# Kernel optimization log

Hardware: AMD Instinct MI355X
Metric: run time of the kernel (lower is better)

## Reference

```python
import jax, jax.numpy as jnp
import numpy as np

IN_FEATS, H_FEATS, OUT_FEATS = 128, 256, 64
N_NODES, N_EDGES = 50000, 800000
DROP_P = 0.5


def setup_inputs() -> dict:
    key = jax.random.key(0)
    k_h, k_e, k_w1, k_w2 = jax.random.split(key, 4)
    h = jax.random.normal(k_h, (N_NODES, IN_FEATS), dtype=jnp.float32)
    edge_index = jax.random.randint(k_e, (2, N_EDGES), 0, N_NODES, dtype=jnp.int64)
    # Glorot-style init for GraphConv weights; bias zeros (DGL default)
    W1 = jax.random.normal(k_w1, (IN_FEATS, H_FEATS), dtype=jnp.float32) / np.sqrt(IN_FEATS)
    b1 = jnp.zeros((H_FEATS,), dtype=jnp.float32)
    W2 = jax.random.normal(k_w2, (H_FEATS, OUT_FEATS), dtype=jnp.float32) / np.sqrt(H_FEATS)
    b2 = jnp.zeros((OUT_FEATS,), dtype=jnp.float32)
    return {"h": h, "W1": W1, "b1": b1, "W2": W2, "b2": b2,
            "edge_index": edge_index, "n_nodes": N_NODES}


def _sym_norm(edge_index, n_nodes):
    # symmetric GCN norm: deg^-1/2 on both endpoints (in-degree, clamped to 1)
    dst = edge_index[1]
    deg = jax.ops.segment_sum(jnp.ones(edge_index.shape[1], jnp.float32), dst,
                              num_segments=n_nodes)
    return jnp.where(deg > 0, deg, 1.0) ** -0.5  # [N]


def _graph_conv(h, W, b, src, dst, norm, n_nodes, apply_w_first):
    # DGL GraphConv (norm='both'): scale by src norm, aggregate, scale by dst norm.
    # W is applied before aggregation if in_feats > out_feats, else after.
    x = h * norm[:, None]
    if apply_w_first:
        x = x @ W
    agg = jax.ops.segment_sum(x[src], dst, num_segments=n_nodes)
    if not apply_w_first:
        agg = agg @ W
    return agg * norm[:, None] + b


def reference(h, W1, b1, W2, b2, edge_index, n_nodes):
    src, dst = edge_index[0], edge_index[1]
    norm = _sym_norm(edge_index, n_nodes)
    # layer 1: in(128) <= out(256) -> aggregate then transform; relu activation
    h1 = jax.nn.relu(_graph_conv(h, W1, b1, src, dst, norm, n_nodes, apply_w_first=False))
    # dropout(0.5), training mode, deterministic key
    keep = jax.random.bernoulli(jax.random.key(42), 1.0 - DROP_P, h1.shape)
    h1 = jnp.where(keep, h1 / (1.0 - DROP_P), 0.0)
    # layer 2: in(256) > out(64) -> transform then aggregate; no activation
    out = _graph_conv(h1, W2, b2, src, dst, norm, n_nodes, apply_w_first=True)
    return out
```

## Files before the change

kernel.cpp:

```cpp
#include <hip/hip_runtime.h>
#include <stdint.h>

#define N_IN  128
#define N_H   256
#define N_OUT 64
#define CHK   2048
#define CAP   6144

typedef __attribute__((ext_vector_type(8))) __bf16 bf16x8;
typedef __attribute__((ext_vector_type(4))) float f32x4;

__device__ __forceinline__ void tf4(uint32_t& x0, uint32_t& x1,
                                    const int r0, const int r1, const int r2, const int r3) {
  x0 += x1; x1 = (x1 << r0) | (x1 >> (32 - r0)); x1 ^= x0;
  x0 += x1; x1 = (x1 << r1) | (x1 >> (32 - r1)); x1 ^= x0;
  x0 += x1; x1 = (x1 << r2) | (x1 >> (32 - r2)); x1 ^= x0;
  x0 += x1; x1 = (x1 << r3) | (x1 >> (32 - r3)); x1 ^= x0;
}

__device__ __forceinline__ uint2 threefry2x32(uint32_t k0, uint32_t k1, uint32_t x0, uint32_t x1) {
  const uint32_t k2 = k0 ^ k1 ^ 0x1BD11BDAu;
  x0 += k0; x1 += k1;
  tf4(x0, x1, 13, 15, 26, 6);   x0 += k1; x1 += k2 + 1u;
  tf4(x0, x1, 17, 29, 16, 24);  x0 += k2; x1 += k0 + 2u;
  tf4(x0, x1, 13, 15, 26, 6);   x0 += k0; x1 += k1 + 3u;
  tf4(x0, x1, 17, 29, 16, 24);  x0 += k1; x1 += k2 + 4u;
  tf4(x0, x1, 13, 15, 26, 6);   x0 += k2; x1 += k0 + 5u;
  return make_uint2(x0, x1);
}

__device__ __forceinline__ uint16_t f2bf_rne(float v) {
  uint32_t b = __builtin_bit_cast(uint32_t, v);
  b += 0x7fffu + ((b >> 16) & 1u);
  return (uint16_t)(b >> 16);
}
__device__ __forceinline__ float bflo(uint32_t w) { return __builtin_bit_cast(float, w << 16); }
__device__ __forceinline__ float bfhi(uint32_t w) { return __builtin_bit_cast(float, w & 0xffff0000u); }

__device__ __forceinline__ void packW_body(const float* __restrict__ W,
                                           uint4* __restrict__ WH, uint4* __restrict__ WL,
                                           int Ncols, int nct, int nks, int g) {
  if (g >= nct * nks * 64) return;
  int lane = g & 63;
  int grp = g >> 6;
  int ks = grp % nks, ct = grp / nks;
  int k0 = ks * 32 + (lane >> 4) * 8;
  int col = ct * 16 + (lane & 15);
  uint32_t hb[8], lb[8];
#pragma unroll
  for (int j = 0; j < 8; j++) {
    float w = W[(size_t)(k0 + j) * Ncols + col];
    uint32_t bits = __builtin_bit_cast(uint32_t, w);
    uint32_t hi = bits & 0xffff0000u;
    float lo = w - __builtin_bit_cast(float, hi);
    hb[j] = hi >> 16;
    lb[j] = __builtin_bit_cast(uint32_t, lo) >> 16;
  }
  WH[g] = make_uint4(hb[0] | (hb[1] << 16), hb[2] | (hb[3] << 16),
                     hb[4] | (hb[5] << 16), hb[6] | (hb[7] << 16));
  WL[g] = make_uint4(lb[0] | (lb[1] << 16), lb[2] | (lb[3] << 16),
                     lb[4] | (lb[5] << 16), lb[6] | (lb[7] << 16));
}

__global__ __launch_bounds__(256) void k_front(
    const int* __restrict__ eidx, int E, int* __restrict__ bktCur, uint2* __restrict__ eb,
    uint16_t* __restrict__ mask, int N,
    const float* __restrict__ W1, uint4* __restrict__ W1H, uint4* __restrict__ W1L,
    const float* __restrict__ W2, uint4* __restrict__ W2H, uint4* __restrict__ W2L,
    int NBE) {
  const int b = blockIdx.x, t = threadIdx.x;
  if (b < NBE) {
    __shared__ int s_nz;
    __shared__ int hist[256];
    __shared__ int base[256];
    if (t == 0) s_nz = 0;
    hist[t] = 0;
    __syncthreads();
    int n = E < 2048 ? E : 2048;
    int nz = 0;
    for (int i = t; i < n; i += 256) nz |= (eidx[2 * i + 1] != 0) ? 1 : 0;
    if (nz) atomicAdd(&s_nz, 1);
    __syncthreads();
    int stride = (s_nz == 0) ? 2 : 1;

    int cb = b * CHK;
    int dc[8], sc[8];
#pragma unroll
    for (int i = 0; i < 8; i++) {
      int e = cb + i * 256 + t;
      if (e < E) {
        dc[i] = eidx[(size_t)(E + e) * stride];
        sc[i] = eidx[(size_t)e * stride];
        atomicAdd(&hist[dc[i] >> 8], 1);
      } else dc[i] = -1;
    }
    __syncthreads();
    int hcnt = hist[t];
    if (hcnt) base[t] = atomicAdd(&bktCur[t], hcnt);
    __syncthreads();
    hist[t] = 0;
    __syncthreads();
#pragma unroll
    for (int i = 0; i < 8; i++) {
      if (dc[i] >= 0) {
        int bk = dc[i] >> 8;
        int r = atomicAdd(&hist[bk], 1);
        eb[(size_t)bk * CAP + base[bk] + r] = make_uint2((unsigned)sc[i], (unsigned)dc[i]);
      }
    }
  } else {
    const int NBM = (N * 16 + 255) >> 8;
    int bb = b - NBE;
    if (bb < NBM) {
      int g = bb * 256 + t;
      if (g >= N * 16) return;
      uint32_t row = (uint32_t)(g >> 4), colb = (uint32_t)(g & 15);
      uint32_t bse = row * 256u + colb;
      uint32_t m = 0;
#pragma unroll
      for (int ct = 0; ct < 16; ct++) {
        uint2 o = threefry2x32(0u, 42u, 0u, bse + (uint32_t)ct * 16u);
        uint32_t bits = o.x ^ o.y;
        m |= ((~bits) >> 31) << ct;
      }
      mask[g] = (uint16_t)m;
    } else if (bb < NBM + 16) {
      packW_body(W1, W1H, W1L, N_H, 16, 4, (bb - NBM) * 256 + t);
    } else {
      packW_body(W2, W2H, W2L, N_OUT, 4, 8, (bb - NBM - 16) * 256 + t);
    }
  }
}

__global__ __launch_bounds__(256) void k_bucket_csr(
    const uint2* __restrict__ eb, const int* __restrict__ bktCur,
    int* __restrict__ rowptr, float* __restrict__ norm,
    int* __restrict__ esrc, int N, int E) {
  __shared__ int s[256];
  __shared__ int cnt[256];
  __shared__ int pfx[256];
  __shared__ int cur[256];
  const int b = blockIdx.x, t = threadIdx.x;
  if (b == 0 && t == 0) rowptr[N] = E;
  if (b * 256 >= N) return;
  int xc = bktCur[t];
  s[t] = xc;
  __syncthreads();
  for (int off = 1; off < 256; off <<= 1) {
    int u = (t >= off) ? s[t - off] : 0;
    __syncthreads();
    s[t] += u;
    __syncthreads();
  }
  const int lo = (b > 0) ? s[b - 1] : 0;
  const int ecnt = s[b] - lo;
  const uint2* ebb = eb + (size_t)b * CAP;
  cnt[t] = 0;
  __syncthreads();
  for (int e = t; e < ecnt; e += 256)
    atomicAdd(&cnt[ebb[e].y & 255u], 1);
  __syncthreads();
  int x = cnt[t];
  pfx[t] = x;
  __syncthreads();
  for (int off = 1; off < 256; off <<= 1) {
    int u = (t >= off) ? pfx[t - off] : 0;
    __syncthreads();
    pfx[t] += u;
    __syncthreads();
  }
  int excl = pfx[t] - x;
  int node = b * 256 + t;
  if (node < N) {
    rowptr[node] = lo + excl;
    norm[node] = x > 0 ? rsqrtf((float)x) : 1.0f;
  }
  cur[t] = excl;
  __syncthreads();
  for (int e = t; e < ecnt; e += 256) {
    uint2 r = ebb[e];
    int d = (int)(r.y & 255u);
    int p = atomicAdd(&cur[d], 1);
    esrc[lo + p] = (int)r.x;
  }
}

__global__ __launch_bounds__(256) void k_mid(
    int* __restrict__ esrc, const int* __restrict__ rowptr, int N,
    const float* __restrict__ h, const float* __restrict__ norm,
    uint16_t* __restrict__ hn, int NS) {
  const int b = blockIdx.x, t = threadIdx.x;
  if (b < NS) {
    int node = b * 4 + (t >> 6);
    if (node >= N) return;
    const int lane = t & 63;
    int lo = rowptr[node], hi = rowptr[node + 1], d = hi - lo;
    if (d <= 1) return;
    if (d <= 64) {
      int v = (lane < d) ? esrc[lo + lane] : 0x7fffffff;
#pragma unroll
      for (int k = 2; k <= 64; k <<= 1) {
#pragma unroll
        for (int j = k >> 1; j > 0; j >>= 1) {
          int other = __shfl_xor(v, j);
          bool up = ((lane & k) == 0);
          bool lower = ((lane & j) == 0);
          int mn = min(v, other), mx = max(v, other);
          v = (up == lower) ? mn : mx;
        }
      }
      if (lane < d) esrc[lo + lane] = v;
    } else if (lane == 0) {
      for (int i = lo + 1; i < hi; i++) {
        int v = esrc[i];
        int j = i - 1;
        while (j >= lo && esrc[j] > v) { esrc[j + 1] = esrc[j]; j--; }
        esrc[j + 1] = v;
      }
    }
  } else {
    int g = (b - NS) * 256 + t;
    if (g >= N * 32) return;
    float nr = norm[g >> 5];
    float4 v = *reinterpret_cast<const float4*>(h + (size_t)g * 4);
    ushort4 r;
    r.x = f2bf_rne(v.x * nr);
    r.y = f2bf_rne(v.y * nr);
    r.z = f2bf_rne(v.z * nr);
    r.w = f2bf_rne(v.w * nr);
    *reinterpret_cast<ushort4*>(hn + (size_t)g * 4) = r;
  }
}

__global__ __launch_bounds__(256) void k_pull1(
    const uint16_t* __restrict__ hn, const int* __restrict__ rowptr,
    const int* __restrict__ esrc, uint16_t* __restrict__ aggB, int N) {
  int node = blockIdx.x * 16 + (threadIdx.x >> 4);
  if (node >= N) return;
  int lane = threadIdx.x & 15;
  int lo = rowptr[node], hi = rowptr[node + 1];
  float a[8] = {0,0,0,0,0,0,0,0};
  float b[8] = {0,0,0,0,0,0,0,0};
  int e = lo;
  for (; e + 7 < hi; e += 8) {
    int s0 = esrc[e],     s1 = esrc[e + 1], s2 = esrc[e + 2], s3 = esrc[e + 3];
    int s4 = esrc[e + 4], s5 = esrc[e + 5], s6 = esrc[e + 6], s7 = esrc[e + 7];
    uint4 v0 = *reinterpret_cast<const uint4*>(hn + (size_t)s0 * N_IN + lane * 8);
    uint4 v1 = *reinterpret_cast<const uint4*>(hn + (size_t)s1 * N_IN + lane * 8);
    uint4 v2 = *reinterpret_cast<const uint4*>(hn + (size_t)s2 * N_IN + lane * 8);
    uint4 v3 = *reinterpret_cast<const uint4*>(hn + (size_t)s3 * N_IN + lane * 8);
    uint4 v4 = *reinterpret_cast<const uint4*>(hn + (size_t)s4 * N_IN + lane * 8);
    uint4 v5 = *reinterpret_cast<const uint4*>(hn + (size_t)s5 * N_IN + lane * 8);
    uint4 v6 = *reinterpret_cast<const uint4*>(hn + (size_t)s6 * N_IN + lane * 8);
    uint4 v7 = *reinterpret_cast<const uint4*>(hn + (size_t)s7 * N_IN + lane * 8);
    a[0] += bflo(v0.x); a[1] += bfhi(v0.x); a[2] += bflo(v0.y); a[3] += bfhi(v0.y);
    a[4] += bflo(v0.z); a[5] += bfhi(v0.z); a[6] += bflo(v0.w); a[7] += bfhi(v0.w);
    b[0] += bflo(v1.x); b[1] += bfhi(v1.x); b[2] += bflo(v1.y); b[3] += bfhi(v1.y);
    b[4] += bflo(v1.z); b[5] += bfhi(v1.z); b[6] += bflo(v1.w); b[7] += bfhi(v1.w);
    a[0] += bflo(v2.x); a[1] += bfhi(v2.x); a[2] += bflo(v2.y); a[3] += bfhi(v2.y);
    a[4] += bflo(v2.z); a[5] += bfhi(v2.z); a[6] += bflo(v2.w); a[7] += bfhi(v2.w);
    b[0] += bflo(v3.x); b[1] += bfhi(v3.x); b[2] += bflo(v3.y); b[3] += bfhi(v3.y);
    b[4] += bflo(v3.z); b[5] += bfhi(v3.z); b[6] += bflo(v3.w); b[7] += bfhi(v3.w);
    a[0] += bflo(v4.x); a[1] += bfhi(v4.x); a[2] += bflo(v4.y); a[3] += bfhi(v4.y);
    a[4] += bflo(v4.z); a[5] += bfhi(v4.z); a[6] += bflo(v4.w); a[7] += bfhi(v4.w);
    b[0] += bflo(v5.x); b[1] += bfhi(v5.x); b[2] += bflo(v5.y); b[3] += bfhi(v5.y);
    b[4] += bflo(v5.z); b[5] += bfhi(v5.z); b[6] += bflo(v5.w); b[7] += bfhi(v5.w);
    a[0] += bflo(v6.x); a[1] += bfhi(v6.x); a[2] += bflo(v6.y); a[3] += bfhi(v6.y);
    a[4] += bflo(v6.z); a[5] += bfhi(v6.z); a[6] += bflo(v6.w); a[7] += bfhi(v6.w);
    b[0] += bflo(v7.x); b[1] += bfhi(v7.x); b[2] += bflo(v7.y); b[3] += bfhi(v7.y);
    b[4] += bflo(v7.z); b[5] += bfhi(v7.z); b[6] += bflo(v7.w); b[7] += bfhi(v7.w);
  }
  for (; e < hi; e++) {
    uint4 v0 = *reinterpret_cast<const uint4*>(hn + (size_t)esrc[e] * N_IN + lane * 8);
    a[0] += bflo(v0.x); a[1] += bfhi(v0.x); a[2] += bflo(v0.y); a[3] += bfhi(v0.y);
    a[4] += bflo(v0.z); a[5] += bfhi(v0.z); a[6] += bflo(v0.w); a[7] += bfhi(v0.w);
  }
  uint16_t o[8];
#pragma unroll
  for (int i = 0; i < 8; i++) o[i] = f2bf_rne(a[i] + b[i]);
  *reinterpret_cast<uint4*>(aggB + (size_t)node * N_IN + lane * 8) =
      *reinterpret_cast<const uint4*>(o);
}

__global__ __launch_bounds__(256) void k_gemm12(
    const uint16_t* __restrict__ aggB,
    const uint4* __restrict__ W1H, const uint4* __restrict__ W1L,
    const float* __restrict__ b1, const float* __restrict__ norm,
    const uint16_t* __restrict__ mask,
    const uint4* __restrict__ W2H, const uint4* __restrict__ W2L,
    uint16_t* __restrict__ zbf, int Nn) {
  __shared__ uint16_t h1[64 * 256];
  __shared__ uint4 wlds[2048];
  const int tid = threadIdx.x;
  const int wave = tid >> 6, lane = tid & 63;
  const int row0 = blockIdx.x * 64 + wave * 16;
  const int lrow = lane & 15, lk = lane >> 4;
  int arow = row0 + lrow; if (arow >= Nn) arow = Nn - 1;

  uint4 aq[4];
#pragma unroll
  for (int ks = 0; ks < 4; ks++)
    aq[ks] = *reinterpret_cast<const uint4*>(aggB + (size_t)arow * N_IN + ks * 32 + lk * 8);

  f32x4 acc[16];
#pragma unroll
  for (int c = 0; c < 16; c++) acc[c] = f32x4{0.f, 0.f, 0.f, 0.f};

  for (int ks = 0; ks < 4; ks++) {
    __syncthreads();
#pragma unroll
    for (int i = 0; i < 4; i++) {
      int g = tid + i * 256;
      int src = ((g >> 6) * 4 + ks) * 64 + (g & 63);
      wlds[g]        = W1H[src];
      wlds[1024 + g] = W1L[src];
    }
    __syncthreads();
    union { uint4 q; bf16x8 v; } ah; ah.q = aq[ks];
#pragma unroll
    for (int c = 0; c < 16; c++) {
      union { uint4 q; bf16x8 v; } bh, bl;
      bh.q = wlds[c * 64 + lane];
      bl.q = wlds[1024 + c * 64 + lane];
      acc[c] = __builtin_amdgcn_mfma_f32_16x16x32_bf16(ah.v, bh.v, acc[c], 0, 0, 0);
      acc[c] = __builtin_amdgcn_mfma_f32_16x16x32_bf16(ah.v, bl.v, acc[c], 0, 0, 0);
    }
  }

  const int colb = lane & 15, rgrp = lane >> 4;
#pragma unroll
  for (int r = 0; r < 4; r++) {
    int lrw = wave * 16 + rgrp * 4 + r;
    int row = blockIdx.x * 64 + lrw;
    float nr = (row < Nn) ? norm[row] : 0.f;
    uint32_t m = (row < Nn) ? (uint32_t)mask[row * 16 + colb] : 0u;
    int sw = (lrw & 7) << 3;
#pragma unroll
    for (int c = 0; c < 16; c++) {
      int col = c * 16 + colb;
      float v = fmaf(acc[c][r], nr, b1[col]);
      v = fmaxf(v, 0.f);
      v = ((m >> c) & 1u) ? v * (2.0f * nr) : 0.f;
      h1[lrw * 256 + (col ^ sw)] = f2bf_rne(v);
    }
  }

  f32x4 acc2[4];
#pragma unroll
  for (int c = 0; c < 4; c++) acc2[c] = f32x4{0.f, 0.f, 0.f, 0.f};
  const int myrow = wave * 16 + lrow;
  const int sw2 = (myrow & 7) << 3;

  for (int half = 0; half < 2; half++) {
    __syncthreads();
#pragma unroll
    for (int i = 0; i < 4; i++) {
      int g = tid + i * 256;
      int src = ((g >> 8) * 8 + half * 4 + ((g >> 6) & 3)) * 64 + (g & 63);
      wlds[g]        = W2H[src];
      wlds[1024 + g] = W2L[src];
    }
    __syncthreads();
#pragma unroll
    for (int ksl = 0; ksl < 4; ksl++) {
      int ks = half * 4 + ksl;
      union { uint4 q; bf16x8 v; } ah;
      int c0 = (ks * 32 + lk * 8) ^ sw2;
      ah.q = *reinterpret_cast<const uint4*>(&h1[myrow * 256 + c0]);
#pragma unroll
      for (int c = 0; c < 4; c++) {
        union { uint4 q; bf16x8 v; } bh, bl;
        bh.q = wlds[(c * 4 + ksl) * 64 + lane];
        bl.q = wlds[1024 + (c * 4 + ksl) * 64 + lane];
        acc2[c] = __builtin_amdgcn_mfma_f32_16x16x32_bf16(ah.v, bh.v, acc2[c], 0, 0, 0);
        acc2[c] = __builtin_amdgcn_mfma_f32_16x16x32_bf16(ah.v, bl.v, acc2[c], 0, 0, 0);
      }
    }
  }
#pragma unroll
  for (int r = 0; r < 4; r++) {
    int row = row0 + rgrp * 4 + r;
    if (row >= Nn) continue;
#pragma unroll
    for (int c = 0; c < 4; c++)
      zbf[(size_t)row * N_OUT + c * 16 + colb] = f2bf_rne(acc2[c][r]);
  }
}

__global__ __launch_bounds__(256) void k_pull2(
    const uint16_t* __restrict__ zbf, const float* __restrict__ norm,
    const float* __restrict__ b2, const int* __restrict__ rowptr,
    const int* __restrict__ esrc, float* __restrict__ out, int N) {
  int node = blockIdx.x * 32 + (threadIdx.x >> 3);
  if (node >= N) return;
  int lane = threadIdx.x & 7;
  int lo = rowptr[node], hi = rowptr[node + 1];
  float a[8] = {0,0,0,0,0,0,0,0};
  float b[8] = {0,0,0,0,0,0,0,0};
  int e = lo;
  for (; e + 7 < hi; e += 8) {
    int s0 = esrc[e],     s1 = esrc[e + 1], s2 = esrc[e + 2], s3 = esrc[e + 3];
    int s4 = esrc[e + 4], s5 = esrc[e + 5], s6 = esrc[e + 6], s7 = esrc[e + 7];
    uint4 v0 = *reinterpret_cast<const uint4*>(zbf + (size_t)s0 * N_OUT + lane * 8);
    uint4 v1 = *reinterpret_cast<const uint4*>(zbf + (size_t)s1 * N_OUT + lane * 8);
    uint4 v2 = *reinterpret_cast<const uint4*>(zbf + (size_t)s2 * N_OUT + lane * 8);
    uint4 v3 = *reinterpret_cast<const uint4*>(zbf + (size_t)s3 * N_OUT + lane * 8);
    uint4 v4 = *reinterpret_cast<const uint4*>(zbf + (size_t)s4 * N_OUT + lane * 8);
    uint4 v5 = *reinterpret_cast<const uint4*>(zbf + (size_t)s5 * N_OUT + lane * 8);
    uint4 v6 = *reinterpret_cast<const uint4*>(zbf + (size_t)s6 * N_OUT + lane * 8);
    uint4 v7 = *reinterpret_cast<const uint4*>(zbf + (size_t)s7 * N_OUT + lane * 8);
    a[0] += bflo(v0.x); a[1] += bfhi(v0.x); a[2] += bflo(v0.y); a[3] += bfhi(v0.y);
    a[4] += bflo(v0.z); a[5] += bfhi(v0.z); a[6] += bflo(v0.w); a[7] += bfhi(v0.w);
    b[0] += bflo(v1.x); b[1] += bfhi(v1.x); b[2] += bflo(v1.y); b[3] += bfhi(v1.y);
    b[4] += bflo(v1.z); b[5] += bfhi(v1.z); b[6] += bflo(v1.w); b[7] += bfhi(v1.w);
    a[0] += bflo(v2.x); a[1] += bfhi(v2.x); a[2] += bflo(v2.y); a[3] += bfhi(v2.y);
    a[4] += bflo(v2.z); a[5] += bfhi(v2.z); a[6] += bflo(v2.w); a[7] += bfhi(v2.w);
    b[0] += bflo(v3.x); b[1] += bfhi(v3.x); b[2] += bflo(v3.y); b[3] += bfhi(v3.y);
    b[4] += bflo(v3.z); b[5] += bfhi(v3.z); b[6] += bflo(v3.w); b[7] += bfhi(v3.w);
    a[0] += bflo(v4.x); a[1] += bfhi(v4.x); a[2] += bflo(v4.y); a[3] += bfhi(v4.y);
    a[4] += bflo(v4.z); a[5] += bfhi(v4.z); a[6] += bflo(v4.w); a[7] += bfhi(v4.w);
    b[0] += bflo(v5.x); b[1] += bfhi(v5.x); b[2] += bflo(v5.y); b[3] += bfhi(v5.y);
    b[4] += bflo(v5.z); b[5] += bfhi(v5.z); b[6] += bflo(v5.w); b[7] += bfhi(v5.w);
    a[0] += bflo(v6.x); a[1] += bfhi(v6.x); a[2] += bflo(v6.y); a[3] += bfhi(v6.y);
    a[4] += bflo(v6.z); a[5] += bfhi(v6.z); a[6] += bflo(v6.w); a[7] += bfhi(v6.w);
    b[0] += bflo(v7.x); b[1] += bfhi(v7.x); b[2] += bflo(v7.y); b[3] += bfhi(v7.y);
    b[4] += bflo(v7.z); b[5] += bfhi(v7.z); b[6] += bflo(v7.w); b[7] += bfhi(v7.w);
  }
  for (; e < hi; e++) {
    uint4 v0 = *reinterpret_cast<const uint4*>(zbf + (size_t)esrc[e] * N_OUT + lane * 8);
    a[0] += bflo(v0.x); a[1] += bfhi(v0.x); a[2] += bflo(v0.y); a[3] += bfhi(v0.y);
    a[4] += bflo(v0.z); a[5] += bfhi(v0.z); a[6] += bflo(v0.w); a[7] += bfhi(v0.w);
  }
  float nn = norm[node];
  float o[8];
#pragma unroll
  for (int i = 0; i < 8; i++) o[i] = (a[i] + b[i]) * nn + b2[lane * 8 + i];
  *reinterpret_cast<float4*>(out + (size_t)node * N_OUT + lane * 8) =
      make_float4(o[0], o[1], o[2], o[3]);
  *reinterpret_cast<float4*>(out + (size_t)node * N_OUT + lane * 8 + 4) =
      make_float4(o[4], o[5], o[6], o[7]);
}

extern "C" void kernel_launch(void* const* d_in, const int* in_sizes, int n_in,
                              void* d_out, int out_size, void* d_ws, size_t ws_size,
                              hipStream_t stream) {
  const float* h  = (const float*)d_in[0];
  const float* W1 = (const float*)d_in[1];
  const float* b1 = (const float*)d_in[2];
  const float* W2 = (const float*)d_in[3];
  const float* b2 = (const float*)d_in[4];
  const int* eidx = (const int*)d_in[5];
  const int N = in_sizes[0] / N_IN;
  const int E = in_sizes[5] / 2;
  const int NBE = (E + CHK - 1) / CHK;
  const int NBM = (N * 16 + 255) / 256;
  const int NS  = (N + 3) / 4;
  const int NH  = (N * 32 + 255) / 256;

  char* ws = (char*)d_ws;
  size_t off = 0;
  auto alloc = [&](size_t bytes) { void* p = ws + off; off += (bytes + 511) & ~(size_t)511; return p; };
  int*      rowptr = (int*)alloc((size_t)(N + 1) * 4);
  float*    norm   = (float*)alloc((size_t)N * 4);
  int*      esrc   = (int*)alloc((size_t)E * 4);
  int*      bktCur = (int*)alloc((size_t)256 * 4);
  uint16_t* mask   = (uint16_t*)alloc((size_t)N * 16 * 2);
  uint4*    W1H    = (uint4*)alloc((size_t)16 * 4 * 64 * 16);
  uint4*    W1L    = (uint4*)alloc((size_t)16 * 4 * 64 * 16);
  uint4*    W2H    = (uint4*)alloc((size_t)4 * 8 * 64 * 16);
  uint4*    W2L    = (uint4*)alloc((size_t)4 * 8 * 64 * 16);
  uint2*    eb     = (uint2*)alloc((size_t)256 * CAP * 8);
  uint16_t* hn     = (uint16_t*)alloc((size_t)N * N_IN * 2);
  uint16_t* aggB   = (uint16_t*)alloc((size_t)N * N_IN * 2);
  uint16_t* zbf    = (uint16_t*)alloc((size_t)N * N_OUT * 2);
  float*    out    = (float*)d_out;

  hipMemsetAsync(bktCur, 0, 256 * 4, stream);

  k_front<<<NBE + NBM + 16 + 8, 256, 0, stream>>>(eidx, E, bktCur, eb,
                                                  mask, N, W1, W1H, W1L, W2, W2H, W2L, NBE);

  k_bucket_csr<<<256, 256, 0, stream>>>(eb, bktCur, rowptr, norm, esrc, N, E);

  k_mid<<<NS + NH, 256, 0, stream>>>(esrc, rowptr, N, h, norm, hn, NS);

  k_pull1<<<(N + 15) / 16, 256, 0, stream>>>(hn, rowptr, esrc, aggB, N);

  k_gemm12<<<(N + 63) / 64, 256, 0, stream>>>(aggB, W1H, W1L, b1, norm, mask,
                                              W2H, W2L, zbf, N);

  k_pull2<<<(N + 31) / 32, 256, 0, stream>>>(zbf, norm, b2, rowptr, esrc, out, N);
}
```

Before: 146.1 us.

## Fuse per-row edge sort and feature normalization into bucket CSR kernel

Drops the separate k_mid kernel. Each bucket block of k_bucket_csr now sorts its own rows' source lists and writes the normalized bf16 features for its 256 nodes, reading counts and norms from shared memory. This removes one launch and the rowptr/norm reloads from global memory. The cost is that the sort and conversion run on only 256 blocks, one wave per 64 rows serially, rather than across many blocks, so parallelism drops sharply.

After: 205.1 us. +40.3%, slower.

```diff
diff --git a/kernel.cpp b/kernel.cpp
--- a/kernel.cpp
+++ b/kernel.cpp
@@ -135,11 +135,13 @@
 __global__ __launch_bounds__(256) void k_bucket_csr(
     const uint2* __restrict__ eb, const int* __restrict__ bktCur,
     int* __restrict__ rowptr, float* __restrict__ norm,
-    int* __restrict__ esrc, int N, int E) {
+    int* __restrict__ esrc, const float* __restrict__ h,
+    uint16_t* __restrict__ hn, int N, int E) {
   __shared__ int s[256];
   __shared__ int cnt[256];
   __shared__ int pfx[256];
   __shared__ int cur[256];
+  __shared__ float narr[256];
   const int b = blockIdx.x, t = threadIdx.x;
   if (b == 0 && t == 0) rowptr[N] = E;
   if (b * 256 >= N) return;
@@ -171,9 +173,11 @@
   }
   int excl = pfx[t] - x;
   int node = b * 256 + t;
+  float nrm = x > 0 ? rsqrtf((float)x) : 1.0f;
+  narr[t] = nrm;
   if (node < N) {
     rowptr[node] = lo + excl;
-    norm[node] = x > 0 ? rsqrtf((float)x) : 1.0f;
+    norm[node] = nrm;
   }
   cur[t] = excl;
   __syncthreads();
@@ -183,52 +187,55 @@
     int p = atomicAdd(&cur[d], 1);
     esrc[lo + p] = (int)r.x;
   }
-}
-
-__global__ __launch_bounds__(256) void k_mid(
-    int* __restrict__ esrc, const int* __restrict__ rowptr, int N,
-    const float* __restrict__ h, const float* __restrict__ norm,
-    uint16_t* __restrict__ hn, int NS) {
-  const int b = blockIdx.x, t = threadIdx.x;
-  if (b < NS) {
-    int node = b * 4 + (t >> 6);
-    if (node >= N) return;
-    const int lane = t & 63;
-    int lo = rowptr[node], hi = rowptr[node + 1], d = hi - lo;
-    if (d <= 1) return;
+  __syncthreads();
+
+  const int wv = t >> 6, ln = t & 63;
+  const int nrows = min(256, N - b * 256);
+  for (int i = 0; i < 64; i++) {
+    int r = wv * 64 + i;
+    if (r >= nrows) break;
+    int d = cnt[r];
+    if (d <= 1) continue;
+    int rl = lo + pfx[r] - d;
     if (d <= 64) {
-      int v = (lane < d) ? esrc[lo + lane] : 0x7fffffff;
+      int v = (ln < d) ? esrc[rl + ln] : 0x7fffffff;
 #pragma unroll
       for (int k = 2; k <= 64; k <<= 1) {
 #pragma unroll
         for (int j = k >> 1; j > 0; j >>= 1) {
           int other = __shfl_xor(v, j);
-          bool up = ((lane & k) == 0);
-          bool lower = ((lane & j) == 0);
+          bool up = ((ln & k) == 0);
+          bool lower = ((ln & j) == 0);
           int mn = min(v, other), mx = max(v, other);
           v = (up == lower) ? mn : mx;
         }
       }
-      if (lane < d) esrc[lo + lane] = v;
-    } else if (lane == 0) {
-      for (int i = lo + 1; i < hi; i++) {
-        int v = esrc[i];
-        int j = i - 1;
-        while (j >= lo && esrc[j] > v) { esrc[j + 1] = esrc[j]; j--; }
+      if (ln < d) esrc[rl + ln] = v;
+    } else if (ln == 0) {
+      for (int ii = rl + 1; ii < rl + d; ii++) {
+        int v = esrc[ii];
+        int j = ii - 1;
+        while (j >= rl && esrc[j] > v) { esrc[j + 1] = esrc[j]; j--; }
         esrc[j + 1] = v;
       }
     }
-  } else {
-    int g = (b - NS) * 256 + t;
-    if (g >= N * 32) return;
-    float nr = norm[g >> 5];
-    float4 v = *reinterpret_cast<const float4*>(h + (size_t)g * 4);
-    ushort4 r;
-    r.x = f2bf_rne(v.x * nr);
-    r.y = f2bf_rne(v.y * nr);
-    r.z = f2bf_rne(v.z * nr);
-    r.w = f2bf_rne(v.w * nr);
-    *reinterpret_cast<ushort4*>(hn + (size_t)g * 4) = r;
+  }
+
+#pragma unroll 4
+  for (int i = 0; i < 32; i++) {
+    int g = i * 256 + t;
+    int r = g >> 5;
+    if (r >= nrows) break;
+    int c4 = g & 31;
+    size_t row = (size_t)(b * 256 + r);
+    float4 v = *reinterpret_cast<const float4*>(h + row * N_IN + c4 * 4);
+    float nr = narr[r];
+    ushort4 o;
+    o.x = f2bf_rne(v.x * nr);
+    o.y = f2bf_rne(v.y * nr);
+    o.z = f2bf_rne(v.z * nr);
+    o.w = f2bf_rne(v.w * nr);
+    *reinterpret_cast<ushort4*>(hn + row * N_IN + c4 * 4) = o;
   }
 }
 
@@ -454,8 +461,6 @@
   const int E = in_sizes[5] / 2;
   const int NBE = (E + CHK - 1) / CHK;
   const int NBM = (N * 16 + 255) / 256;
-  const int NS  = (N + 3) / 4;
-  const int NH  = (N * 32 + 255) / 256;
 
   char* ws = (char*)d_ws;
   size_t off = 0;
@@ -480,9 +485,7 @@
   k_front<<<NBE + NBM + 16 + 8, 256, 0, stream>>>(eidx, E, bktCur, eb,
                                                   mask, N, W1, W1H, W1L, W2, W2H, W2L, NBE);
 
-  k_bucket_csr<<<256, 256, 0, stream>>>(eb, bktCur, rowptr, norm, esrc, N, E);
-
-  k_mid<<<NS + NH, 256, 0, stream>>>(esrc, rowptr, N, h, norm, hn, NS);
+  k_bucket_csr<<<256, 256, 0, stream>>>(eb, bktCur, rowptr, norm, esrc, h, hn, N, E);
 
   k_pull1<<<(N + 15) / 16, 256, 0, stream>>>(hn, rowptr, esrc, aggB, N);
 
```
